# Kernel optimization log

Hardware: AMD Instinct MI355X
Metric: run time of the kernel (lower is better)

The kernel has to match this reference:

```python
import jax, jax.numpy as jnp
import numpy as np

DIM = 2048
NUM_HEADS = 16
HEAD_DIM = DIM // NUM_HEADS  # 128


def setup_inputs() -> dict:
    key = jax.random.key(0)
    ks = jax.random.split(key, 5)
    scale = 0.02
    x = jax.random.normal(ks[0], (1, 2048, DIM), dtype=jnp.float32)
    # nn.Linear weights stored as [out_features, in_features]
    Wq = jax.random.normal(ks[1], (DIM, DIM), dtype=jnp.float32) * scale
    Wk = jax.random.normal(ks[2], (HEAD_DIM, DIM), dtype=jnp.float32) * scale
    Wv = jax.random.normal(ks[3], (HEAD_DIM, DIM), dtype=jnp.float32) * scale
    Wo = jax.random.normal(ks[4], (DIM, DIM), dtype=jnp.float32) * scale
    return {"x": x, "Wq": Wq, "Wk": Wk, "Wv": Wv, "Wo": Wo}


def reference(x, Wq, Wk, Wv, Wo):
    batch, seq_len, dim = x.shape
    q = x @ Wq.T                                   # [b, s, dim]
    k = x @ Wk.T                                   # [b, s, head_dim] (shared across heads)
    v = x @ Wv.T                                   # [b, s, head_dim]
    q = q.reshape(batch, seq_len, NUM_HEADS, HEAD_DIM).transpose(0, 2, 1, 3)  # [b, h, s, d]
    # MQA: single KV head broadcast across query heads (no materialized repeat)
    scores = jnp.einsum("bhqd,bkd->bhqk", q, k) / (HEAD_DIM ** 0.5)
    probs = jax.nn.softmax(scores, axis=-1)        # [b, h, q, k]
    out = jnp.einsum("bhqk,bkd->bhqd", probs, v)   # [b, h, s, d]
    out = out.transpose(0, 2, 1, 3).reshape(batch, seq_len, dim)
    return out @ Wo.T
```

## Files before the change

### kernel.cpp

```cpp
#include <hip/hip_runtime.h>
#include <cmath>

typedef float  float4_t __attribute__((ext_vector_type(4)));
typedef __bf16 bf16x8   __attribute__((ext_vector_type(8)));
typedef unsigned short u16;

__device__ __forceinline__ u16 f2bf(float f) {
    unsigned u = __float_as_uint(f);
    u += 0x7fffu + ((u >> 16) & 1u);
    return (u16)(u >> 16);
}
__device__ __forceinline__ u16 f2bf_hu(float f) {
    return (u16)((__float_as_uint(f) + 0x8000u) >> 16);
}

#define GLOAD_LDS16(g, l)                                              \
    __builtin_amdgcn_global_load_lds(                                  \
        (__attribute__((address_space(1))) void*)(g),                  \
        (__attribute__((address_space(3))) void*)(l), 16, 0, 0)

__device__ __forceinline__ int sw_st(int cs, int row) { return ((cs - (row >> 1)) & 3) * 8; }
__device__ __forceinline__ int sw_rd(int quad, int row) { return (((quad + (row >> 1)) & 3)) * 8; }

__global__ __launch_bounds__(256) void cast_all(const float* __restrict__ x,
                                                const float* __restrict__ wq,
                                                const float* __restrict__ wk,
                                                const float* __restrict__ wv,
                                                const float* __restrict__ wo,
                                                u16* __restrict__ xb, u16* __restrict__ wqb,
                                                u16* __restrict__ wkb, u16* __restrict__ wvb,
                                                u16* __restrict__ wob) {
    const int b = blockIdx.x;
    const float* src;
    u16* dst;
    int i;
    if (b < 4096)      { src = x;  dst = xb;  i = b * 256 + threadIdx.x; }
    else if (b < 8192) { src = wq; dst = wqb; i = (b - 4096) * 256 + threadIdx.x; }
    else if (b < 8448) { src = wk; dst = wkb; i = (b - 8192) * 256 + threadIdx.x; }
    else if (b < 8704) { src = wv; dst = wvb; i = (b - 8448) * 256 + threadIdx.x; }
    else               { src = wo; dst = wob; i = (b - 8704) * 256 + threadIdx.x; }
    float4 f = ((const float4*)src)[i];
    ushort4 r;
    r.x = f2bf(f.x); r.y = f2bf(f.y); r.z = f2bf(f.z); r.w = f2bf(f.w);
    ((ushort4*)dst)[i] = r;
}

template <typename EPI>
__device__ __forceinline__ void gemm_core(const u16* __restrict__ A,
                                          const u16* __restrict__ B,
                                          int K, int bm, int bn, EPI epi) {
    __shared__ __align__(16) u16 As[2 * 64 * 32];
    __shared__ __align__(16) u16 Bs[2 * 128 * 32];
    const int tid  = threadIdx.x;
    const int lane = tid & 63, wave = tid >> 6;
    const int quad = lane >> 4, l16 = lane & 15;

    float4_t acc[4][2] = {};

    for (int k0 = 0; k0 < K; k0 += 64) {
#pragma unroll
        for (int i = 0; i < 2; ++i) {
            const int slot = i * 256 + tid;
            const int ks = slot >> 8, win = slot & 255;
            const int row = win >> 2;
            GLOAD_LDS16(A + (size_t)(bm + row) * K + k0 + ks * 32 + sw_st(win & 3, row),
                        &As[slot * 8]);
        }
#pragma unroll
        for (int i = 0; i < 4; ++i) {
            const int slot = i * 256 + tid;
            const int ks = slot >> 9, win = slot & 511;
            const int row = win >> 2;
            GLOAD_LDS16(B + (size_t)(bn + row) * K + k0 + ks * 32 + sw_st(win & 3, row),
                        &Bs[slot * 8]);
        }
        __syncthreads();

        bf16x8 af[2][4], bfr[2][2];
#pragma unroll
        for (int ks = 0; ks < 2; ++ks) {
#pragma unroll
            for (int mi = 0; mi < 4; ++mi) {
                const int rw = mi * 16 + l16;
                af[ks][mi] = *(const bf16x8*)&As[ks * 2048 + rw * 32 + sw_rd(quad, rw)];
            }
#pragma unroll
            for (int ni = 0; ni < 2; ++ni) {
                const int rw = wave * 32 + ni * 16 + l16;
                bfr[ks][ni] = *(const bf16x8*)&Bs[ks * 4096 + rw * 32 + sw_rd(quad, rw)];
            }
        }
#pragma unroll
        for (int mi = 0; mi < 4; ++mi)
#pragma unroll
            for (int ni = 0; ni < 2; ++ni) {
                acc[mi][ni] = __builtin_amdgcn_mfma_f32_16x16x32_bf16(
                    af[0][mi], bfr[0][ni], acc[mi][ni], 0, 0, 0);
                acc[mi][ni] = __builtin_amdgcn_mfma_f32_16x16x32_bf16(
                    af[1][mi], bfr[1][ni], acc[mi][ni], 0, 0, 0);
            }
        __syncthreads();
    }

#pragma unroll
    for (int mi = 0; mi < 4; ++mi) {
        const int row = bm + mi * 16 + quad * 4;
#pragma unroll
        for (int ni = 0; ni < 2; ++ni) {
            const int col = bn + wave * 32 + ni * 16 + l16;
#pragma unroll
            for (int r = 0; r < 4; ++r) epi(row + r, col, acc[mi][ni][r]);
        }
    }
}

__global__ __launch_bounds__(256) void gemm_qkv(const u16* __restrict__ A,
                                                const u16* __restrict__ B,
                                                u16* __restrict__ qb,
                                                u16* __restrict__ kb,
                                                u16* __restrict__ vtb) {
    gemm_core(A, B, 2048, blockIdx.x * 64, blockIdx.y * 128,
              [=](int row, int col, float v) {
                  if (col < 2048)
                      qb[(size_t)row * 2048 + col] = f2bf(v * 0.1275174313451427f);
                  else if (col < 2176)
                      kb[(size_t)row * 128 + (col - 2048)] = f2bf(v);
                  else
                      vtb[(size_t)(col - 2176) * 2048 + row] = f2bf(v);
              });
}

__global__ __launch_bounds__(256) void gemm_out(const u16* __restrict__ A,
                                                const u16* __restrict__ B,
                                                float* __restrict__ C) {
    gemm_core(A, B, 2048, blockIdx.x * 64, blockIdx.y * 128,
              [=](int row, int col, float v) {
                  C[(size_t)row * 2048 + col] = v;
              });
}

__global__ __launch_bounds__(256) void mqa_attn(const u16* __restrict__ Q,
                                                const u16* __restrict__ Kmat,
                                                const u16* __restrict__ Vt,
                                                float* __restrict__ Oacc0,
                                                float* __restrict__ Oacc1,
                                                float* __restrict__ Lsum) {
    __shared__ __align__(16) u16 Ks[4 * 64 * 32];
    __shared__ __align__(16) u16 Vts[2 * 128 * 32];
    __shared__ __align__(16) u16 Ps[4][32 * 72];
    const int tid  = threadIdx.x;
    const int wave = tid >> 6, lane = tid & 63;
    const int quad = lane >> 4, l16 = lane & 15;
    const int h     = blockIdx.y;
    const int ks    = blockIdx.z;
    const int qbase = blockIdx.x * 128 + wave * 32;
    const int kbase = ks * 1024;

    bf16x8 qf[2][4];
#pragma unroll
    for (int mt = 0; mt < 2; ++mt)
#pragma unroll
        for (int kb4 = 0; kb4 < 4; ++kb4)
            qf[mt][kb4] = *(const bf16x8*)(Q + (size_t)(qbase + mt * 16 + l16) * 2048 +
                                           h * 128 + kb4 * 32 + quad * 8);

    float4_t acc[2][8];
#pragma unroll
    for (int mt = 0; mt < 2; ++mt)
#pragma unroll
        for (int nt = 0; nt < 8; ++nt) acc[mt][nt] = (float4_t){0.f, 0.f, 0.f, 0.f};
    float lsum[8] = {};

    u16* pb = Ps[wave];

    for (int s = 0; s < 16; ++s) {
        const int k0 = kbase + s * 64;
#pragma unroll
        for (int i = 0; i < 4; ++i) {
            const int slot = i * 256 + tid;
            const int kb4 = slot >> 8, win = slot & 255;
            const int row = win >> 2;
            GLOAD_LDS16(Kmat + (size_t)(k0 + row) * 128 + kb4 * 32 + sw_st(win & 3, row),
                        &Ks[slot * 8]);
        }
#pragma unroll
        for (int i = 0; i < 4; ++i) {
            const int slot = i * 256 + tid;
            const int kk = slot >> 9, win = slot & 511;
            const int row = win >> 2;
            GLOAD_LDS16(Vt + (size_t)row * 2048 + k0 + kk * 32 + sw_st(win & 3, row),
                        &Vts[slot * 8]);
        }
        __syncthreads();

#pragma unroll
        for (int ct = 0; ct < 4; ++ct) {
            float4_t s0 = (float4_t){0.f, 0.f, 0.f, 0.f};
            float4_t s1 = (float4_t){0.f, 0.f, 0.f, 0.f};
#pragma unroll
            for (int kb4 = 0; kb4 < 4; ++kb4) {
                const int rw = ct * 16 + l16;
                bf16x8 kf = *(const bf16x8*)&Ks[kb4 * 2048 + rw * 32 + sw_rd(quad, rw)];
                s0 = __builtin_amdgcn_mfma_f32_16x16x32_bf16(qf[0][kb4], kf, s0, 0, 0, 0);
                s1 = __builtin_amdgcn_mfma_f32_16x16x32_bf16(qf[1][kb4], kf, s1, 0, 0, 0);
            }
#pragma unroll
            for (int r = 0; r < 4; ++r) {
                const float e0 = exp2f(s0[r]);
                const float e1 = exp2f(s1[r]);
                lsum[r]     += e0;
                lsum[4 + r] += e1;
                pb[(quad * 4 + r) * 72 + ct * 16 + l16]      = f2bf_hu(e0);
                pb[(16 + quad * 4 + r) * 72 + ct * 16 + l16] = f2bf_hu(e1);
            }
        }
        bf16x8 pa[2][2];
#pragma unroll
        for (int mt = 0; mt < 2; ++mt)
#pragma unroll
            for (int kk = 0; kk < 2; ++kk)
                pa[mt][kk] = *(const bf16x8*)&pb[(mt * 16 + l16) * 72 + kk * 32 + quad * 8];
#pragma unroll
        for (int kk = 0; kk < 2; ++kk)
#pragma unroll
            for (int nt = 0; nt < 8; ++nt) {
                const int rw = nt * 16 + l16;
                bf16x8 vf = *(const bf16x8*)&Vts[kk * 4096 + rw * 32 + sw_rd(quad, rw)];
                acc[0][nt] = __builtin_amdgcn_mfma_f32_16x16x32_bf16(pa[0][kk], vf, acc[0][nt], 0, 0, 0);
                acc[1][nt] = __builtin_amdgcn_mfma_f32_16x16x32_bf16(pa[1][kk], vf, acc[1][nt], 0, 0, 0);
            }
        __syncthreads();
    }

    float* __restrict__ Op = ks ? Oacc1 : Oacc0;
#pragma unroll
    for (int mt = 0; mt < 2; ++mt)
#pragma unroll
        for (int r = 0; r < 4; ++r) {
            const int row = qbase + mt * 16 + quad * 4 + r;
            const size_t base = ((size_t)h * 2048 + row) * 128;
            float lrow = lsum[mt * 4 + r];
#pragma unroll
            for (int off = 1; off < 16; off <<= 1) lrow += __shfl_xor(lrow, off);
            if (l16 == 0) Lsum[(size_t)ks * 32768 + h * 2048 + row] = lrow;
#pragma unroll
            for (int nt = 0; nt < 8; ++nt)
                Op[base + nt * 16 + l16] = acc[mt][nt][r];
        }
}

__global__ __launch_bounds__(256) void attn_combine(const float* __restrict__ O0,
                                                    const float* __restrict__ O1,
                                                    const float* __restrict__ L,
                                                    u16* __restrict__ attn) {
    const int f = blockIdx.x * 256 + threadIdx.x;
    const int d4 = f & 31, h = (f >> 5) & 15, q = f >> 9;
    const int li = h * 2048 + q;
    const float inv = 1.0f / (L[li] + L[32768 + li]);
    const int oi = li * 32 + d4;
    const float4 a = ((const float4*)O0)[oi];
    const float4 b = ((const float4*)O1)[oi];
    ushort4 r;
    r.x = f2bf((a.x + b.x) * inv);
    r.y = f2bf((a.y + b.y) * inv);
    r.z = f2bf((a.z + b.z) * inv);
    r.w = f2bf((a.w + b.w) * inv);
    ((ushort4*)attn)[f] = r;
}

extern "C" void kernel_launch(void* const* d_in, const int* in_sizes, int n_in,
                              void* d_out, int out_size, void* d_ws, size_t ws_size,
                              hipStream_t stream) {
    const float* x  = (const float*)d_in[0];
    const float* Wq = (const float*)d_in[1];
    const float* Wk = (const float*)d_in[2];
    const float* Wv = (const float*)d_in[3];
    const float* Wo = (const float*)d_in[4];
    float* out = (float*)d_out;

    u16* ws   = (u16*)d_ws;
    u16* xb   = ws;
    u16* Wqb  = xb  + (4 << 20);
    u16* Wkb  = Wqb + (4 << 20);
    u16* Wvb  = Wkb + (256 << 10);
    u16* Wob  = Wvb + (256 << 10);
    u16* qb   = Wob + (4 << 20);
    u16* kb   = qb  + (4 << 20);
    u16* vtb  = kb  + (256 << 10);
    u16* attn = vtb + (256 << 10);
    float* Oacc0 = (float*)ws;
    float* Oacc1 = (float*)(attn + (4 << 20));
    float* Lsum  = Oacc1 + (4 << 20);

    cast_all<<<12800, 256, 0, stream>>>(x, Wq, Wk, Wv, Wo, xb, Wqb, Wkb, Wvb, Wob);

    gemm_qkv<<<dim3(32, 18), 256, 0, stream>>>(xb, Wqb, qb, kb, vtb);
    mqa_attn<<<dim3(16, 16, 2), 256, 0, stream>>>(qb, kb, vtb, Oacc0, Oacc1, Lsum);
    attn_combine<<<4096, 256, 0, stream>>>(Oacc0, Oacc1, Lsum, attn);
    gemm_out<<<dim3(32, 16), 256, 0, stream>>>(attn, Wob, out);
}
```

Before: 226.7 us.

## Use 128x128 GEMM tiles with 32x32x16 MFMA and 2x2 wave layout

The shared GEMM core now computes 128x128 output tiles instead of 64x128, arranges the four waves in a 2x2 grid with 64x64 sub-tiles each, and switches from 16x16x32 to 32x32x16 bf16 MFMA with 16-float accumulators. The larger tile and larger MFMA shape raise arithmetic intensity and cut LDS reads per flop. In exchange the GEMM launch grids are halved (288 and 256 blocks), which may underfill the GPU's compute units, and per-thread accumulator register use goes up. The epilogue store pattern also changes to follow the 32x32 accumulator layout.

```diff
diff --git a/kernel.cpp b/kernel.cpp
--- a/kernel.cpp
+++ b/kernel.cpp
@@ -1,8 +1,9 @@
 #include <hip/hip_runtime.h>
 #include <cmath>
 
-typedef float  float4_t __attribute__((ext_vector_type(4)));
-typedef __bf16 bf16x8   __attribute__((ext_vector_type(8)));
+typedef float  float4_t  __attribute__((ext_vector_type(4)));
+typedef float  float16_t __attribute__((ext_vector_type(16)));
+typedef __bf16 bf16x8    __attribute__((ext_vector_type(8)));
 typedef unsigned short u16;
 
 __device__ __forceinline__ u16 f2bf(float f) {
@@ -20,7 +21,7 @@
         (__attribute__((address_space(3))) void*)(l), 16, 0, 0)
 
 __device__ __forceinline__ int sw_st(int cs, int row) { return ((cs - (row >> 1)) & 3) * 8; }
-__device__ __forceinline__ int sw_rd(int quad, int row) { return (((quad + (row >> 1)) & 3)) * 8; }
+__device__ __forceinline__ int sw_rdc(int c, int row) { return (((c + (row >> 1)) & 3)) * 8; }
 
 __global__ __launch_bounds__(256) void cast_all(const float* __restrict__ x,
                                                 const float* __restrict__ wq,
@@ -49,69 +50,64 @@
 __device__ __forceinline__ void gemm_core(const u16* __restrict__ A,
                                           const u16* __restrict__ B,
                                           int K, int bm, int bn, EPI epi) {
-    __shared__ __align__(16) u16 As[2 * 64 * 32];
+    __shared__ __align__(16) u16 As[2 * 128 * 32];
     __shared__ __align__(16) u16 Bs[2 * 128 * 32];
     const int tid  = threadIdx.x;
     const int lane = tid & 63, wave = tid >> 6;
-    const int quad = lane >> 4, l16 = lane & 15;
-
-    float4_t acc[4][2] = {};
+    const int wm = wave >> 1, wn = wave & 1;
+    const int l32 = lane & 31, lh = lane >> 5;
+
+    float16_t acc[2][2] = {};
 
     for (int k0 = 0; k0 < K; k0 += 64) {
-#pragma unroll
-        for (int i = 0; i < 2; ++i) {
-            const int slot = i * 256 + tid;
-            const int ks = slot >> 8, win = slot & 255;
-            const int row = win >> 2;
-            GLOAD_LDS16(A + (size_t)(bm + row) * K + k0 + ks * 32 + sw_st(win & 3, row),
-                        &As[slot * 8]);
-        }
 #pragma unroll
         for (int i = 0; i < 4; ++i) {
             const int slot = i * 256 + tid;
             const int ks = slot >> 9, win = slot & 511;
             const int row = win >> 2;
+            GLOAD_LDS16(A + (size_t)(bm + row) * K + k0 + ks * 32 + sw_st(win & 3, row),
+                        &As[slot * 8]);
             GLOAD_LDS16(B + (size_t)(bn + row) * K + k0 + ks * 32 + sw_st(win & 3, row),
                         &Bs[slot * 8]);
         }
         __syncthreads();
 
-        bf16x8 af[2][4], bfr[2][2];
-#pragma unroll
-        for (int ks = 0; ks < 2; ++ks) {
-#pragma unroll
-            for (int mi = 0; mi < 4; ++mi) {
-                const int rw = mi * 16 + l16;
-                af[ks][mi] = *(const bf16x8*)&As[ks * 2048 + rw * 32 + sw_rd(quad, rw)];
-            }
-#pragma unroll
-            for (int ni = 0; ni < 2; ++ni) {
-                const int rw = wave * 32 + ni * 16 + l16;
-                bfr[ks][ni] = *(const bf16x8*)&Bs[ks * 4096 + rw * 32 + sw_rd(quad, rw)];
-            }
-        }
-#pragma unroll
-        for (int mi = 0; mi < 4; ++mi)
-#pragma unroll
-            for (int ni = 0; ni < 2; ++ni) {
-                acc[mi][ni] = __builtin_amdgcn_mfma_f32_16x16x32_bf16(
-                    af[0][mi], bfr[0][ni], acc[mi][ni], 0, 0, 0);
-                acc[mi][ni] = __builtin_amdgcn_mfma_f32_16x16x32_bf16(
-                    af[1][mi], bfr[1][ni], acc[mi][ni], 0, 0, 0);
-            }
+#pragma unroll
+        for (int kc = 0; kc < 4; ++kc) {
+            const int ks = kc >> 1;
+            const int c  = (kc & 1) * 2 + lh;
+            bf16x8 af[2], bfr[2];
+#pragma unroll
+            for (int mt = 0; mt < 2; ++mt) {
+                const int rw = wm * 64 + mt * 32 + l32;
+                af[mt] = *(const bf16x8*)&As[ks * 4096 + rw * 32 + sw_rdc(c, rw)];
+            }
+#pragma unroll
+            for (int nt = 0; nt < 2; ++nt) {
+                const int rw = wn * 64 + nt * 32 + l32;
+                bfr[nt] = *(const bf16x8*)&Bs[ks * 4096 + rw * 32 + sw_rdc(c, rw)];
+            }
+#pragma unroll
+            for (int mt = 0; mt < 2; ++mt)
+#pragma unroll
+                for (int nt = 0; nt < 2; ++nt)
+                    acc[mt][nt] = __builtin_amdgcn_mfma_f32_32x32x16_bf16(
+                        af[mt], bfr[nt], acc[mt][nt], 0, 0, 0);
+        }
         __syncthreads();
     }
 
 #pragma unroll
-    for (int mi = 0; mi < 4; ++mi) {
-        const int row = bm + mi * 16 + quad * 4;
-#pragma unroll
-        for (int ni = 0; ni < 2; ++ni) {
-            const int col = bn + wave * 32 + ni * 16 + l16;
-#pragma unroll
-            for (int r = 0; r < 4; ++r) epi(row + r, col, acc[mi][ni][r]);
-        }
-    }
+    for (int mt = 0; mt < 2; ++mt)
+#pragma unroll
+        for (int nt = 0; nt < 2; ++nt) {
+            const int colg = bn + wn * 64 + nt * 32 + l32;
+#pragma unroll
+            for (int reg = 0; reg < 16; ++reg) {
+                const int rowl = (reg & 3) + 8 * (reg >> 2) + 4 * lh;
+                epi(bm + wm * 64 + mt * 32 + rowl, colg, acc[mt][nt][reg]);
+            }
+        }
 }
 
 __global__ __launch_bounds__(256) void gemm_qkv(const u16* __restrict__ A,
@@ -119,7 +115,7 @@
                                                 u16* __restrict__ qb,
                                                 u16* __restrict__ kb,
                                                 u16* __restrict__ vtb) {
-    gemm_core(A, B, 2048, blockIdx.x * 64, blockIdx.y * 128,
+    gemm_core(A, B, 2048, blockIdx.x * 128, blockIdx.y * 128,
               [=](int row, int col, float v) {
                   if (col < 2048)
                       qb[(size_t)row * 2048 + col] = f2bf(v * 0.1275174313451427f);
@@ -133,7 +129,7 @@
 __global__ __launch_bounds__(256) void gemm_out(const u16* __restrict__ A,
                                                 const u16* __restrict__ B,
                                                 float* __restrict__ C) {
-    gemm_core(A, B, 2048, blockIdx.x * 64, blockIdx.y * 128,
+    gemm_core(A, B, 2048, blockIdx.x * 128, blockIdx.y * 128,
               [=](int row, int col, float v) {
                   C[(size_t)row * 2048 + col] = v;
               });
@@ -200,7 +196,7 @@
 #pragma unroll
             for (int kb4 = 0; kb4 < 4; ++kb4) {
                 const int rw = ct * 16 + l16;
-                bf16x8 kf = *(const bf16x8*)&Ks[kb4 * 2048 + rw * 32 + sw_rd(quad, rw)];
+                bf16x8 kf = *(const bf16x8*)&Ks[kb4 * 2048 + rw * 32 + sw_rdc(quad, rw)];
                 s0 = __builtin_amdgcn_mfma_f32_16x16x32_bf16(qf[0][kb4], kf, s0, 0, 0, 0);
                 s1 = __builtin_amdgcn_mfma_f32_16x16x32_bf16(qf[1][kb4], kf, s1, 0, 0, 0);
             }
@@ -225,7 +221,7 @@
 #pragma unroll
             for (int nt = 0; nt < 8; ++nt) {
                 const int rw = nt * 16 + l16;
-                bf16x8 vf = *(const bf16x8*)&Vts[kk * 4096 + rw * 32 + sw_rd(quad, rw)];
+                bf16x8 vf = *(const bf16x8*)&Vts[kk * 4096 + rw * 32 + sw_rdc(quad, rw)];
                 acc[0][nt] = __builtin_amdgcn_mfma_f32_16x16x32_bf16(pa[0][kk], vf, acc[0][nt], 0, 0, 0);
                 acc[1][nt] = __builtin_amdgcn_mfma_f32_16x16x32_bf16(pa[1][kk], vf, acc[1][nt], 0, 0, 0);
             }
@@ -294,8 +290,8 @@
 
     cast_all<<<12800, 256, 0, stream>>>(x, Wq, Wk, Wv, Wo, xb, Wqb, Wkb, Wvb, Wob);
 
-    gemm_qkv<<<dim3(32, 18), 256, 0, stream>>>(xb, Wqb, qb, kb, vtb);
+    gemm_qkv<<<dim3(16, 18), 256, 0, stream>>>(xb, Wqb, qb, kb, vtb);
     mqa_attn<<<dim3(16, 16, 2), 256, 0, stream>>>(qb, kb, vtb, Oacc0, Oacc1, Lsum);
     attn_combine<<<4096, 256, 0, stream>>>(Oacc0, Oacc1, Lsum, attn);
-    gemm_out<<<dim3(32, 16), 256, 0, stream>>>(attn, Wob, out);
-}
+    gemm_out<<<dim3(16, 16), 256, 0, stream>>>(attn, Wob, out);
+}
```

Result: slower. 238.9 us (+5.4%).
